# Kernel tuning notes

Hardware: AMD Instinct MI355X
Metric: run time of the kernel (lower is better)

Reference implementation:

```python
import jax, jax.numpy as jnp
import numpy as np

VOXEL_SIZE = np.array([0.32, 0.32, 6.0], dtype=np.float32)
SPATIAL_SIZE = np.array([-74.88, 74.88, -74.88, 74.88, -3.0, 3.0], dtype=np.float32)
# voxel_spatial_size = ceil((max-min)/voxel_size) per dim -> [468, 468, 1]
GRID = np.array([int(np.ceil((SPATIAL_SIZE[2*i+1]-SPATIAL_SIZE[2*i])/VOXEL_SIZE[i])) for i in range(3)], dtype=np.int32)
# voxel origin = floor(min / voxel_size) -> [-234, -234, -1]
ORIGIN = np.floor(SPATIAL_SIZE[0::2] / VOXEL_SIZE).astype(np.int32)
VOL = int(np.prod(GRID))  # 468*468*1
# row-major id multipliers: prods[1:]+[1] -> [468, 1, 1]
SHIFT = np.array([int(np.prod(GRID[1:])), int(np.prod(GRID[2:])), 1], dtype=np.int32)
VOXEL_FEATURE_MIN = -1000.0

B, N, D_IN, MLP = 4, 100000, 16, 128


def setup_inputs() -> dict:
    key = jax.random.key(0)
    k1, k2, k3, k4, k5 = jax.random.split(key, 5)
    xy = jax.random.uniform(k1, (B, N, 2), minval=-80.0, maxval=80.0)
    z = jax.random.uniform(k2, (B, N, 1), minval=-4.0, maxval=4.0)
    point_xyz = jnp.concatenate([xy, z], axis=-1)
    point_feature = jax.random.normal(k3, (B, N, D_IN), dtype=jnp.float32)
    point_mask = jax.random.uniform(k4, (B, N)) < 0.95
    W = jax.random.normal(k5, (D_IN + 3, MLP), dtype=jnp.float32) * 0.1
    b = jnp.zeros((MLP,), dtype=jnp.float32)
    return {"point_xyz": point_xyz, "point_feature": point_feature,
            "point_mask": point_mask, "W": W, "b": b}


def reference(point_xyz, point_feature, point_mask, W, b):
    vs = jnp.asarray(VOXEL_SIZE, dtype=point_xyz.dtype)
    # PointToVoxel
    pvx_f = jnp.floor(point_xyz / vs)                      # [B,N,3] float voxel coords
    point_voxel_feature = point_xyz - pvx_f * vs           # delta within voxel
    pvx = pvx_f.astype(jnp.int32) - jnp.asarray(ORIGIN)    # shifted int voxel coords
    grid = jnp.asarray(GRID)
    in_bounds = jnp.all((pvx >= 0) & (pvx < grid), axis=-1)
    voxel_mask = in_bounds & point_mask                    # [B,N]
    vid = jnp.sum(pvx * jnp.asarray(SHIFT), axis=-1)       # [B,N]
    vid = vid + jnp.arange(B, dtype=jnp.int32)[:, None] * VOL
    vid = vid * voxel_mask.astype(jnp.int32)               # invalid -> 0
    # point net (Dense + ReLU) on [point_feature, voxel delta]
    feat = jnp.concatenate([point_feature, point_voxel_feature], axis=-1)
    mf = voxel_mask.astype(feat.dtype)[..., None]
    feat = feat * mf
    feat = jax.nn.relu(jnp.einsum('bnd,dk->bnk', feat, W) + b)
    feat = feat * mf
    # scatter-max into dense voxel grid
    seg = jax.ops.segment_max(feat.reshape(-1, MLP), vid.reshape(-1),
                              num_segments=B * VOL)
    seg = jnp.where(seg > VOXEL_FEATURE_MIN, seg, 0.0)
    # z dim is 1 -> squeezed: [B, 468, 468, MLP]
    return seg.reshape(B, int(GRID[0]), int(GRID[1]), MLP)
```

## Files before the change

### kernel.cpp

```cpp
#include <hip/hip_runtime.h>
#include <hip/hip_bf16.h>
#include <stdint.h>

#define BB   4
#define NN   100000
#define TOTAL (BB * NN)
#define DIN  16
#define DF   19
#define KO   128
#define GX   468
#define GY   468
#define VOL  (GX * GY)
#define NV   (BB * VOL)
#define CAP  12
#define SLOT_F 20
#define NWAVES (NV / 64)

typedef float vfloat2 __attribute__((ext_vector_type(2)));

#define WS_COUNTS   0
#define WS_FLAG     (NV)
#define WS_PACKED   (NV + 16)

__global__ __launch_bounds__(256) void prep(
    int4* __restrict__ counts4,
    const uint4* __restrict__ mask_words,
    int* __restrict__ flag)
{
    if (blockIdx.x == 0) {
        __shared__ int sA, sB;
        if (threadIdx.x == 0) { sA = 0; sB = 0; }
        __syncthreads();
        int a = 0, b = 0;
        #pragma unroll
        for (int it = 0; it < 4; ++it) {
            uint4 w = mask_words[it * 256 + threadIdx.x];
            unsigned lo = (w.x & 0xFFu) | (w.y & 0xFFu) | (w.z & 0xFFu) | (w.w & 0xFFu);
            unsigned hi = (w.x & 0xFFFFFF00u) | (w.y & 0xFFFFFF00u) |
                          (w.z & 0xFFFFFF00u) | (w.w & 0xFFFFFF00u);
            if (hi) a = 1;
            if (lo) b = 1;
        }
        if (a) atomicOr(&sA, 1);
        if (b) atomicOr(&sB, 1);
        __syncthreads();
        if (threadIdx.x == 0) flag[0] = (sA && sB) ? 1 : 4;
    }
    const int i = blockIdx.x * 256 + threadIdx.x;
    if (i < NV / 4) counts4[i] = make_int4(0, 0, 0, 0);
}

__global__ __launch_bounds__(256) void pass1_bin(
    const float* __restrict__ xyz,
    const float* __restrict__ pfeat,
    const unsigned char* __restrict__ mask_raw,
    const int* __restrict__ flag,
    int* __restrict__ counts,
    float* __restrict__ packed)
{
    const int p = blockIdx.x * 256 + threadIdx.x;
    if (p >= TOTAL) return;
    const float x = xyz[p * 3 + 0];
    const float y = xyz[p * 3 + 1];
    const float z = xyz[p * 3 + 2];
    bool m;
    if (flag[0] == 4) m = (((const int*)mask_raw)[p] != 0);
    else              m = (mask_raw[p] != 0);
    const float fx = floorf(x / 0.32f);
    const float fy = floorf(y / 0.32f);
    const float fz = floorf(z / 6.0f);
    const int ix = (int)fx + 234;
    const int iy = (int)fy + 234;
    const int iz = (int)fz + 1;
    const bool inb = ((unsigned)ix < (unsigned)GX) &
                     ((unsigned)iy < (unsigned)GY) &
                     (iz == 0) & m;
    if (!inb) return;
    const int vid = (p / NN) * VOL + ix * GY + iy;
    const int rank = atomicAdd(&counts[vid], 1);
    if (rank >= CAP) return;

    float4* slot = (float4*)(packed + (size_t)(vid * CAP + rank) * SLOT_F);
    const float4* pf4 = (const float4*)(pfeat + (size_t)p * DIN);
    slot[0] = pf4[0];
    slot[1] = pf4[1];
    slot[2] = pf4[2];
    slot[3] = pf4[3];
    slot[4] = make_float4(x - fx * 0.32f, y - fy * 0.32f, z - fz * 6.0f, 0.f);
}

__global__ __launch_bounds__(256) void fused_write(
    const float* __restrict__ W,
    const float* __restrict__ bias,
    const int* __restrict__ counts,
    const float* __restrict__ packed,
    float* __restrict__ out)
{
    const int lane = threadIdx.x & 63;
    const int wid  = (blockIdx.x * 256 + threadIdx.x) >> 6;
    if (wid >= NWAVES) return;
    const int v0 = wid * 64;

    const int c_mine = counts[v0 + lane];
    const unsigned long long occ = __ballot(c_mine > 0);

    const float2* W2 = (const float2*)W;
    float2 w[DF];
    #pragma unroll
    for (int d = 0; d < DF; ++d) w[d] = W2[d * 64 + lane];
    const float2 bb = ((const float2*)bias)[lane];

    vfloat2* dst0 = (vfloat2*)(out + (size_t)v0 * KO) + lane;

    {
        vfloat2 zz = {0.f, 0.f};
        unsigned long long emp = ~occ;
        while (emp) {
            const int j = __builtin_ctzll(emp);
            emp &= emp - 1;
            __builtin_nontemporal_store(zz, dst0 + (size_t)j * 64);
        }
    }

    unsigned long long rem = occ;
    int j_cur = -1;
    float4 q0, q1, q2, q3, q4;
    if (rem) {
        j_cur = __builtin_ctzll(rem);
        rem &= rem - 1;
        const float4* base = (const float4*)(packed +
                             (size_t)(v0 + j_cur) * CAP * SLOT_F);
        q0 = base[0]; q1 = base[1]; q2 = base[2]; q3 = base[3]; q4 = base[4];
    }
    while (j_cur >= 0) {
        int j_nxt = -1;
        float4 n0, n1, n2, n3, n4;
        if (rem) {
            j_nxt = __builtin_ctzll(rem);
            rem &= rem - 1;
            const float4* nb = (const float4*)(packed +
                               (size_t)(v0 + j_nxt) * CAP * SLOT_F);
            n0 = nb[0]; n1 = nb[1]; n2 = nb[2]; n3 = nb[3]; n4 = nb[4];
        }

        const int c = min(__shfl(c_mine, j_cur), CAP);
        const float4* base = (const float4*)(packed +
                             (size_t)(v0 + j_cur) * CAP * SLOT_F);
        float m0 = -3.0e38f, m1 = -3.0e38f;
        for (int t = 0; t < c; ++t) {
            float4 p0, p1, p2, p3, p4;
            if (t == 0) { p0 = q0; p1 = q1; p2 = q2; p3 = q3; p4 = q4; }
            else {
                p0 = base[t * 5 + 0]; p1 = base[t * 5 + 1];
                p2 = base[t * 5 + 2]; p3 = base[t * 5 + 3];
                p4 = base[t * 5 + 4];
            }
            float a0 = bb.x, a1 = bb.y;
            a0 = fmaf(p0.x, w[0].x, a0);  a1 = fmaf(p0.x, w[0].y, a1);
            a0 = fmaf(p0.y, w[1].x, a0);  a1 = fmaf(p0.y, w[1].y, a1);
            a0 = fmaf(p0.z, w[2].x, a0);  a1 = fmaf(p0.z, w[2].y, a1);
            a0 = fmaf(p0.w, w[3].x, a0);  a1 = fmaf(p0.w, w[3].y, a1);
            a0 = fmaf(p1.x, w[4].x, a0);  a1 = fmaf(p1.x, w[4].y, a1);
            a0 = fmaf(p1.y, w[5].x, a0);  a1 = fmaf(p1.y, w[5].y, a1);
            a0 = fmaf(p1.z, w[6].x, a0);  a1 = fmaf(p1.z, w[6].y, a1);
            a0 = fmaf(p1.w, w[7].x, a0);  a1 = fmaf(p1.w, w[7].y, a1);
            a0 = fmaf(p2.x, w[8].x, a0);  a1 = fmaf(p2.x, w[8].y, a1);
            a0 = fmaf(p2.y, w[9].x, a0);  a1 = fmaf(p2.y, w[9].y, a1);
            a0 = fmaf(p2.z, w[10].x, a0); a1 = fmaf(p2.z, w[10].y, a1);
            a0 = fmaf(p2.w, w[11].x, a0); a1 = fmaf(p2.w, w[11].y, a1);
            a0 = fmaf(p3.x, w[12].x, a0); a1 = fmaf(p3.x, w[12].y, a1);
            a0 = fmaf(p3.y, w[13].x, a0); a1 = fmaf(p3.y, w[13].y, a1);
            a0 = fmaf(p3.z, w[14].x, a0); a1 = fmaf(p3.z, w[14].y, a1);
            a0 = fmaf(p3.w, w[15].x, a0); a1 = fmaf(p3.w, w[15].y, a1);
            a0 = fmaf(p4.x, w[16].x, a0); a1 = fmaf(p4.x, w[16].y, a1);
            a0 = fmaf(p4.y, w[17].x, a0); a1 = fmaf(p4.y, w[17].y, a1);
            a0 = fmaf(p4.z, w[18].x, a0); a1 = fmaf(p4.z, w[18].y, a1);
            m0 = fmaxf(m0, a0);
            m1 = fmaxf(m1, a1);
        }
        vfloat2 rv = {fmaxf(m0, 0.f), fmaxf(m1, 0.f)};
        __builtin_nontemporal_store(rv, dst0 + (size_t)j_cur * 64);

        j_cur = j_nxt;
        q0 = n0; q1 = n1; q2 = n2; q3 = n3; q4 = n4;
    }
}

extern "C" void kernel_launch(void* const* d_in, const int* in_sizes, int n_in,
                              void* d_out, int out_size, void* d_ws, size_t ws_size,
                              hipStream_t stream) {
    const float* xyz   = (const float*)d_in[0];
    const float* pfeat = (const float*)d_in[1];
    const unsigned char* mask = (const unsigned char*)d_in[2];
    const float* W     = (const float*)d_in[3];
    const float* bias  = (const float*)d_in[4];
    float* out = (float*)d_out;
    int* ws = (int*)d_ws;

    int*   counts = ws + WS_COUNTS;
    int*   flag   = ws + WS_FLAG;
    float* packed = (float*)(ws + WS_PACKED);

    prep<<<(NV / 4 + 255) / 256, 256, 0, stream>>>((int4*)counts,
                                                   (const uint4*)mask, flag);
    pass1_bin<<<(TOTAL + 255) / 256, 256, 0, stream>>>(xyz, pfeat, mask, flag,
                                                       counts, packed);
    fused_write<<<(NWAVES + 3) / 4, 256, 0, stream>>>(W, bias, counts,
                                                      packed, out);
}
```

Before: 536.4 us.

## Zero-fill entire output in prep kernel, write only occupied voxels later

Moves zeroing of the dense output grid into the prep kernel as a grid-stride float4 fill, alongside the counts clear. The write kernel now skips empty-voxel stores entirely and exits early for waves with no occupied voxels. This aims for a more coalesced streaming fill but writes occupied voxels twice, adding extra output traffic.

```diff
diff --git a/kernel.cpp b/kernel.cpp
--- a/kernel.cpp
+++ b/kernel.cpp
@@ -1,5 +1,4 @@
 #include <hip/hip_runtime.h>
-#include <hip/hip_bf16.h>
 #include <stdint.h>
 
 #define BB   4
@@ -15,6 +14,7 @@
 #define CAP  12
 #define SLOT_F 20
 #define NWAVES (NV / 64)
+#define OUT_F4 ((size_t)NV * KO / 4)
 
 typedef float vfloat2 __attribute__((ext_vector_type(2)));
 
@@ -22,7 +22,8 @@
 #define WS_FLAG     (NV)
 #define WS_PACKED   (NV + 16)
 
-__global__ __launch_bounds__(256) void prep(
+__global__ __launch_bounds__(256) void fill_prep(
+    float4* __restrict__ out4,
     int4* __restrict__ counts4,
     const uint4* __restrict__ mask_words,
     int* __restrict__ flag)
@@ -46,8 +47,12 @@
         __syncthreads();
         if (threadIdx.x == 0) flag[0] = (sA && sB) ? 1 : 4;
     }
-    const int i = blockIdx.x * 256 + threadIdx.x;
-    if (i < NV / 4) counts4[i] = make_int4(0, 0, 0, 0);
+    const unsigned t0 = blockIdx.x * 256 + threadIdx.x;
+    const unsigned stride = gridDim.x * 256;
+    const int4 zi = make_int4(0, 0, 0, 0);
+    for (unsigned i = t0; i < NV / 4; i += stride) counts4[i] = zi;
+    const float4 zf = make_float4(0.f, 0.f, 0.f, 0.f);
+    for (size_t i = t0; i < OUT_F4; i += stride) out4[i] = zf;
 }
 
 __global__ __launch_bounds__(256) void pass1_bin(
@@ -89,7 +94,7 @@
     slot[4] = make_float4(x - fx * 0.32f, y - fy * 0.32f, z - fz * 6.0f, 0.f);
 }
 
-__global__ __launch_bounds__(256) void fused_write(
+__global__ __launch_bounds__(256) void write_occ(
     const float* __restrict__ W,
     const float* __restrict__ bias,
     const int* __restrict__ counts,
@@ -103,6 +108,7 @@
 
     const int c_mine = counts[v0 + lane];
     const unsigned long long occ = __ballot(c_mine > 0);
+    if (!occ) return;
 
     const float2* W2 = (const float2*)W;
     float2 w[DF];
@@ -112,22 +118,11 @@
 
     vfloat2* dst0 = (vfloat2*)(out + (size_t)v0 * KO) + lane;
 
+    unsigned long long rem = occ;
+    int j_cur = __builtin_ctzll(rem);
+    rem &= rem - 1;
+    float4 q0, q1, q2, q3, q4;
     {
-        vfloat2 zz = {0.f, 0.f};
-        unsigned long long emp = ~occ;
-        while (emp) {
-            const int j = __builtin_ctzll(emp);
-            emp &= emp - 1;
-            __builtin_nontemporal_store(zz, dst0 + (size_t)j * 64);
-        }
-    }
-
-    unsigned long long rem = occ;
-    int j_cur = -1;
-    float4 q0, q1, q2, q3, q4;
-    if (rem) {
-        j_cur = __builtin_ctzll(rem);
-        rem &= rem - 1;
         const float4* base = (const float4*)(packed +
                              (size_t)(v0 + j_cur) * CAP * SLOT_F);
         q0 = base[0]; q1 = base[1]; q2 = base[2]; q3 = base[3]; q4 = base[4];
@@ -201,10 +196,10 @@
     int*   flag   = ws + WS_FLAG;
     float* packed = (float*)(ws + WS_PACKED);
 
-    prep<<<(NV / 4 + 255) / 256, 256, 0, stream>>>((int4*)counts,
-                                                   (const uint4*)mask, flag);
+    fill_prep<<<2048, 256, 0, stream>>>((float4*)out, (int4*)counts,
+                                        (const uint4*)mask, flag);
     pass1_bin<<<(TOTAL + 255) / 256, 256, 0, stream>>>(xyz, pfeat, mask, flag,
                                                        counts, packed);
-    fused_write<<<(NWAVES + 3) / 4, 256, 0, stream>>>(W, bias, counts,
-                                                      packed, out);
-}
+    write_occ<<<(NWAVES + 3) / 4, 256, 0, stream>>>(W, bias, counts,
+                                                    packed, out);
+}
```

New measurement: 554.5 us. +3.4%, slower.
